# Performance work log

Hardware: AMD Instinct MI355X
Metric: run time of the kernel (lower is better)

## Reference

```python
import jax, jax.numpy as jnp
import numpy as np

D = 32
H = 64
B, N, M = 2, 512, 512


def setup_inputs() -> dict:
    key = jax.random.key(0)
    ks = jax.random.split(key, 6)
    s = 0.1  # modest init scale for MLP params
    return {
        "Q": jax.random.normal(ks[0], (B, N, D), dtype=jnp.float32),
        "K": jax.random.normal(ks[1], (B, M, D), dtype=jnp.float32),
        "w1": jax.random.normal(ks[2], (D, H), dtype=jnp.float32) * s,
        "b1": jax.random.normal(ks[3], (H,), dtype=jnp.float32) * s,
        "w2": jax.random.normal(ks[4], (H, D * D), dtype=jnp.float32) * s,
        "b2": jax.random.normal(ks[5], (D * D,), dtype=jnp.float32) * s,
    }


def _cholesky_factor(x, w1, b1, w2, b2):
    """L(x) with unit-ish softplus diagonal; x: [..., D] -> L: [..., D, D]."""
    h = jax.nn.silu(x @ w1 + b1)
    raw = h @ w2 + b2                      # [..., D*D]
    raw = 5.0 * jnp.tanh(raw / 5.0)        # soft clamp
    L = (raw + jnp.eye(D, dtype=x.dtype).reshape(-1)).reshape(x.shape[:-1] + (D, D))
    tril = jnp.tril(jnp.ones((D, D), dtype=x.dtype))
    diag = jnp.eye(D, dtype=x.dtype)
    L = L * tril
    L = L * (1.0 - diag) + (jax.nn.softplus(L) + 1e-4) * diag
    return L


def reference(Q, K, w1, b1, w2, b2):
    L_q = _cholesky_factor(Q, w1, b1, w2, b2)   # [B,N,D,D]
    L_k = _cholesky_factor(K, w1, b1, w2, b2)   # [B,M,D,D]
    delta = Q[:, :, None, :] - K[:, None, :, :]  # [B,N,M,D]
    # delta^T G_avg delta = 0.5 (||L_q^T delta||^2 + ||L_k^T delta||^2)
    vq = jnp.einsum('bnij,bnmi->bnmj', L_q, delta)  # L_q^T delta
    vk = jnp.einsum('bmij,bnmi->bnmj', L_k, delta)  # L_k^T delta
    dist_sq = 0.5 * (jnp.sum(vq * vq, axis=-1) + jnp.sum(vk * vk, axis=-1))
    return jnp.sqrt(jnp.clip(dist_sq, 1e-6, 1e6))
```

## Files before the change

kernel.cpp:

```cpp
#include <hip/hip_runtime.h>
#include <math.h>

namespace {
constexpr int KF  = 1152;
constexpr int RPB = 4;
}

typedef __bf16 v8bf __attribute__((ext_vector_type(8)));
typedef float  v4f  __attribute__((ext_vector_type(4)));

__device__ __forceinline__ unsigned short f2bf(float f) {
    union { float f; unsigned u; } v; v.f = f;
    unsigned r = v.u + 0x7FFFu + ((v.u >> 16) & 1u);
    return (unsigned short)(r >> 16);
}

__device__ __forceinline__ v8bf as_v8bf(uint4 u) {
    union { uint4 u; v8bf b; } c; c.u = u; return c.b;
}

__global__ __launch_bounds__(256) void k_feat(
    const float* __restrict__ Q, const float* __restrict__ K,
    const float* __restrict__ w1, const float* __restrict__ b1,
    const float* __restrict__ w2, const float* __restrict__ b2,
    unsigned short* __restrict__ featA, unsigned short* __restrict__ featB,
    float* __restrict__ cOut)
{
    __shared__ __attribute__((aligned(16))) float x_s[RPB][32];
    __shared__ __attribute__((aligned(16))) float h_s[RPB][64];
    __shared__ __attribute__((aligned(16))) float L_s[RPB][32][36];
    __shared__ __attribute__((aligned(16))) float G_s[RPB][528];
    __shared__ __attribute__((aligned(16))) float u_s[RPB][32];
    __shared__ unsigned short tri_s[528];

    const int t  = threadIdx.x;
    const int g0 = blockIdx.x * RPB;

    for (int pr = t; pr < 528; pr += 256) {
        int j = (int)((65.0f - sqrtf(4225.0f - 8.0f * (float)pr)) * 0.5f);
        while (j > 0 && j * (65 - j) / 2 > pr) --j;
        while ((j + 1) * (64 - j) / 2 <= pr) ++j;
        int i = j + (pr - j * (65 - j) / 2);
        tri_s[pr] = (unsigned short)((i << 8) | j);
    }
    if (t < RPB * 32) {
        int r = t >> 5, i = t & 31;
        int g = g0 + r;
        const float* src = (g < 1024) ? (Q + (size_t)g * 32)
                                      : (K + (size_t)(g - 1024) * 32);
        x_s[r][i] = src[i];
    }
    __syncthreads();

    {
        int r = t >> 6, j = t & 63;
        float z = b1[j];
        #pragma unroll
        for (int i = 0; i < 32; ++i) z = fmaf(x_s[r][i], w1[i * 64 + j], z);
        h_s[r][j] = z / (1.0f + __expf(-z));
    }
    __syncthreads();

    {
        const int p4 = t * 4;
        float acc[RPB][4];
        float4 bq = *(const float4*)&b2[p4];
        #pragma unroll
        for (int r = 0; r < RPB; ++r) {
            acc[r][0] = bq.x; acc[r][1] = bq.y; acc[r][2] = bq.z; acc[r][3] = bq.w;
        }
        for (int jb = 0; jb < 8; ++jb) {
            float h8[RPB][8];
            #pragma unroll
            for (int r = 0; r < RPB; ++r) {
                *(float4*)&h8[r][0] = *(const float4*)&h_s[r][jb * 8 + 0];
                *(float4*)&h8[r][4] = *(const float4*)&h_s[r][jb * 8 + 4];
            }
            #pragma unroll
            for (int jj = 0; jj < 8; ++jj) {
                float4 w = *(const float4*)&w2[(size_t)(jb * 8 + jj) * 1024 + p4];
                #pragma unroll
                for (int r = 0; r < RPB; ++r) {
                    acc[r][0] = fmaf(h8[r][jj], w.x, acc[r][0]);
                    acc[r][1] = fmaf(h8[r][jj], w.y, acc[r][1]);
                    acc[r][2] = fmaf(h8[r][jj], w.z, acc[r][2]);
                    acc[r][3] = fmaf(h8[r][jj], w.w, acc[r][3]);
                }
            }
        }
        const int i  = p4 >> 5;
        const int j0 = p4 & 31;
        #pragma unroll
        for (int r = 0; r < RPB; ++r) {
            float4 lv;
            float* lvp = (float*)&lv;
            #pragma unroll
            for (int e = 0; e < 4; ++e) {
                int j = j0 + e;
                float raw = acc[r][e];
                float ex = __expf(0.4f * raw);
                float c5 = 5.0f * (ex - 1.0f) / (ex + 1.0f);
                float val;
                if (i < j)       val = 0.0f;
                else if (i == j) { float z = c5 + 1.0f; val = log1pf(__expf(z)) + 1e-4f; }
                else             val = c5;
                lvp[e] = val;
            }
            *(float4*)&L_s[r][i][j0] = lv;
        }
    }
    __syncthreads();

    for (int idx = t; idx < RPB * 528; idx += 256) {
        int r  = idx / 528;
        int pr = idx - r * 528;
        int tv = tri_s[pr];
        int i = tv >> 8, j = tv & 255;
        const float* Li = &L_s[r][i][0];
        const float* Lj = &L_s[r][j][0];
        float s = 0.0f;
        int nf = (j + 1) >> 2;
        for (int q = 0; q < nf; ++q) {
            float4 a  = *(const float4*)&Li[q * 4];
            float4 bb = *(const float4*)&Lj[q * 4];
            s += a.x * bb.x + a.y * bb.y + a.z * bb.z + a.w * bb.w;
        }
        for (int tt = nf * 4; tt <= j; ++tt) s = fmaf(Li[tt], Lj[tt], s);
        G_s[r][pr] = s;
    }
    __syncthreads();

    if (t < RPB * 32) {
        int r = t >> 5, i = t & 31;
        float s = 0.0f;
        #pragma unroll
        for (int j = 0; j < 32; ++j) {
            float gv = (j <= i) ? G_s[r][j * (65 - j) / 2 + i - j]
                                : G_s[r][i * (65 - i) / 2 + j - i];
            s = fmaf(gv, x_s[r][j], s);
        }
        u_s[r][i] = s;
    }
    __syncthreads();

    if (t < RPB) {
        float s = 0.0f;
        #pragma unroll
        for (int i = 0; i < 32; ++i) s = fmaf(u_s[t][i], x_s[t][i], s);
        cOut[g0 + t] = s;
    }

    for (int idx = t; idx < RPB * (KF / 4); idx += 256) {
        int r   = idx / (KF / 4);
        int q   = idx - r * (KF / 4);
        int pos = q * 4;
        int g   = g0 + r;
        bool isA = (g < 1024);
        unsigned short* dst = isA ? (featA + (size_t)g * KF)
                                  : (featB + (size_t)(g - 1024) * KF);
        unsigned short ev[4];
        #pragma unroll
        for (int e = 0; e < 4; ++e) {
            int p = pos + e;
            float va;
            if (p < 1056) {
                int pr = (p < 528) ? p : p - 528;
                bool wantG = (p < 528) ? isA : !isA;
                int tv = tri_s[pr];
                int i = tv >> 8, j = tv & 255;
                float gv = G_s[r][pr] * ((i == j) ? 1.0f : 2.0f);
                float ov = x_s[r][i] * x_s[r][j];
                va = wantG ? gv : ov;
            } else if (p < 1088) {
                int i = p - 1056;
                va = isA ? u_s[r][i] : -2.0f * x_s[r][i];
            } else if (p < 1120) {
                int i = p - 1088;
                va = isA ? x_s[r][i] : -2.0f * u_s[r][i];
            } else {
                va = 0.0f;
            }
            ev[e] = f2bf(va);
        }
        uint2 w;
        w.x = (unsigned)ev[0] | ((unsigned)ev[1] << 16);
        w.y = (unsigned)ev[2] | ((unsigned)ev[3] << 16);
        *(uint2*)(dst + pos) = w;
    }
}

__global__ __launch_bounds__(64) void k_gemm(
    const unsigned short* __restrict__ featA,
    const unsigned short* __restrict__ featB,
    const float* __restrict__ cOut,
    float* __restrict__ out)
{
    const int lane = threadIdx.x;
    const int m0 = blockIdx.x * 32;
    const int n0 = blockIdx.y * 32;
    const int b  = blockIdx.z;
    const int fr = lane & 15;
    const int fq = lane >> 4;

    const unsigned short* pA0 = featA + (size_t)(b * 512 + n0 + fr) * KF + fq * 8;
    const unsigned short* pA1 = pA0 + (size_t)16 * KF;
    const unsigned short* pB0 = featB + (size_t)(b * 512 + m0 + fr) * KF + fq * 8;
    const unsigned short* pB1 = pB0 + (size_t)16 * KF;

    v4f acc00 = {0,0,0,0}, acc01 = {0,0,0,0}, acc10 = {0,0,0,0}, acc11 = {0,0,0,0};

    uint4 bA0[3], bA1[3], bB0[3], bB1[3];
    #pragma unroll
    for (int s = 0; s < 3; ++s) {
        bA0[s] = *(const uint4*)(pA0 + s * 32);
        bA1[s] = *(const uint4*)(pA1 + s * 32);
        bB0[s] = *(const uint4*)(pB0 + s * 32);
        bB1[s] = *(const uint4*)(pB1 + s * 32);
    }

    for (int ks = 0; ks < 36; ks += 3) {
        #pragma unroll
        for (int s = 0; s < 3; ++s) {
            v8bf a0  = as_v8bf(bA0[s]);
            v8bf a1  = as_v8bf(bA1[s]);
            v8bf b0v = as_v8bf(bB0[s]);
            v8bf b1v = as_v8bf(bB1[s]);
            int kn = ks + s + 3;
            if (kn < 36) {
                bA0[s] = *(const uint4*)(pA0 + kn * 32);
                bA1[s] = *(const uint4*)(pA1 + kn * 32);
                bB0[s] = *(const uint4*)(pB0 + kn * 32);
                bB1[s] = *(const uint4*)(pB1 + kn * 32);
            }
            acc00 = __builtin_amdgcn_mfma_f32_16x16x32_bf16(a0, b0v, acc00, 0, 0, 0);
            acc01 = __builtin_amdgcn_mfma_f32_16x16x32_bf16(a0, b1v, acc01, 0, 0, 0);
            acc10 = __builtin_amdgcn_mfma_f32_16x16x32_bf16(a1, b0v, acc10, 0, 0, 0);
            acc11 = __builtin_amdgcn_mfma_f32_16x16x32_bf16(a1, b1v, acc11, 0, 0, 0);
        }
    }

    const int colm = lane & 15;
    const float cB_0 = cOut[1024 + b * 512 + m0 + colm];
    const float cB_1 = cOut[1024 + b * 512 + m0 + 16 + colm];
    const int rbase = lane >> 4;
    #pragma unroll
    for (int v = 0; v < 4; ++v) {
        int n_lo = n0 + rbase * 4 + v;
        int n_hi = n_lo + 16;
        float cA_lo = cOut[b * 512 + n_lo];
        float cA_hi = cOut[b * 512 + n_hi];
        float vv[4] = { acc00[v], acc01[v], acc10[v], acc11[v] };
        int   nn[4] = { n_lo, n_lo, n_hi, n_hi };
        int   mm[4] = { m0 + colm, m0 + 16 + colm, m0 + colm, m0 + 16 + colm };
        float cc[4] = { cA_lo + cB_0, cA_lo + cB_1, cA_hi + cB_0, cA_hi + cB_1 };
        #pragma unroll
        for (int e = 0; e < 4; ++e) {
            float dsq = 0.5f * (vv[e] + cc[e]);
            dsq = fminf(fmaxf(dsq, 1e-6f), 1e6f);
            out[((size_t)(b * 512 + nn[e])) * 512 + mm[e]] = sqrtf(dsq);
        }
    }
}

extern "C" void kernel_launch(void* const* d_in, const int* in_sizes, int n_in,
                              void* d_out, int out_size, void* d_ws, size_t ws_size,
                              hipStream_t stream)
{
    const float* Q  = (const float*)d_in[0];
    const float* K  = (const float*)d_in[1];
    const float* w1 = (const float*)d_in[2];
    const float* b1 = (const float*)d_in[3];
    const float* w2 = (const float*)d_in[4];
    const float* b2 = (const float*)d_in[5];
    float* out = (float*)d_out;

    unsigned short* featA = (unsigned short*)d_ws;
    unsigned short* featB = featA + (size_t)1024 * KF;
    float* cOut = (float*)(featB + (size_t)1024 * KF);

    k_feat<<<dim3(2048 / RPB), dim3(256), 0, stream>>>(Q, K, w1, b1, w2, b2, featA, featB, cOut);
    k_gemm<<<dim3(16, 16, 2), dim3(64), 0, stream>>>(featA, featB, cOut, out);
}
```

Measured before the change: 103.9 us.

## Split K across four waves per block with LDS reduction and swizzled tiles

```diff
diff --git a/kernel.cpp b/kernel.cpp
--- a/kernel.cpp
+++ b/kernel.cpp
@@ -189,77 +189,100 @@
     }
 }
 
-__global__ __launch_bounds__(64) void k_gemm(
+__global__ __launch_bounds__(256) void k_gemm(
     const unsigned short* __restrict__ featA,
     const unsigned short* __restrict__ featB,
     const float* __restrict__ cOut,
     float* __restrict__ out)
 {
-    const int lane = threadIdx.x;
-    const int m0 = blockIdx.x * 32;
-    const int n0 = blockIdx.y * 32;
-    const int b  = blockIdx.z;
+    __shared__ __attribute__((aligned(16))) float red[4][32][36];
+
+    const int t    = threadIdx.x;
+    const int lane = t & 63;
+    const int w    = t >> 6;
+
+    const int lin = blockIdx.x;
+    const int swz = (lin & 7) * 64 + (lin >> 3);
+    const int m0 = (swz & 15) * 32;
+    const int n0 = ((swz >> 4) & 15) * 32;
+    const int b  = swz >> 8;
+
     const int fr = lane & 15;
     const int fq = lane >> 4;
-
-    const unsigned short* pA0 = featA + (size_t)(b * 512 + n0 + fr) * KF + fq * 8;
+    const int kbase = w * 288 + fq * 8;
+
+    const unsigned short* pA0 = featA + (size_t)(b * 512 + n0 + fr) * KF + kbase;
     const unsigned short* pA1 = pA0 + (size_t)16 * KF;
-    const unsigned short* pB0 = featB + (size_t)(b * 512 + m0 + fr) * KF + fq * 8;
+    const unsigned short* pB0 = featB + (size_t)(b * 512 + m0 + fr) * KF + kbase;
     const unsigned short* pB1 = pB0 + (size_t)16 * KF;
 
     v4f acc00 = {0,0,0,0}, acc01 = {0,0,0,0}, acc10 = {0,0,0,0}, acc11 = {0,0,0,0};
 
-    uint4 bA0[3], bA1[3], bB0[3], bB1[3];
+    uint4 bA0[4], bA1[4], bB0[4], bB1[4];
     #pragma unroll
-    for (int s = 0; s < 3; ++s) {
+    for (int s = 0; s < 4; ++s) {
         bA0[s] = *(const uint4*)(pA0 + s * 32);
         bA1[s] = *(const uint4*)(pA1 + s * 32);
         bB0[s] = *(const uint4*)(pB0 + s * 32);
         bB1[s] = *(const uint4*)(pB1 + s * 32);
     }
 
-    for (int ks = 0; ks < 36; ks += 3) {
-        #pragma unroll
-        for (int s = 0; s < 3; ++s) {
-            v8bf a0  = as_v8bf(bA0[s]);
-            v8bf a1  = as_v8bf(bA1[s]);
-            v8bf b0v = as_v8bf(bB0[s]);
-            v8bf b1v = as_v8bf(bB1[s]);
-            int kn = ks + s + 3;
-            if (kn < 36) {
-                bA0[s] = *(const uint4*)(pA0 + kn * 32);
-                bA1[s] = *(const uint4*)(pA1 + kn * 32);
-                bB0[s] = *(const uint4*)(pB0 + kn * 32);
-                bB1[s] = *(const uint4*)(pB1 + kn * 32);
-            }
-            acc00 = __builtin_amdgcn_mfma_f32_16x16x32_bf16(a0, b0v, acc00, 0, 0, 0);
-            acc01 = __builtin_amdgcn_mfma_f32_16x16x32_bf16(a0, b1v, acc01, 0, 0, 0);
-            acc10 = __builtin_amdgcn_mfma_f32_16x16x32_bf16(a1, b0v, acc10, 0, 0, 0);
-            acc11 = __builtin_amdgcn_mfma_f32_16x16x32_bf16(a1, b1v, acc11, 0, 0, 0);
-        }
-    }
-
-    const int colm = lane & 15;
-    const float cB_0 = cOut[1024 + b * 512 + m0 + colm];
-    const float cB_1 = cOut[1024 + b * 512 + m0 + 16 + colm];
-    const int rbase = lane >> 4;
+    #pragma unroll
+    for (int s = 0; s < 9; ++s) {
+        const int slot = s & 3;
+        v8bf a0  = as_v8bf(bA0[slot]);
+        v8bf a1  = as_v8bf(bA1[slot]);
+        v8bf b0v = as_v8bf(bB0[slot]);
+        v8bf b1v = as_v8bf(bB1[slot]);
+        const int kn = s + 4;
+        if (kn < 9) {
+            bA0[slot] = *(const uint4*)(pA0 + kn * 32);
+            bA1[slot] = *(const uint4*)(pA1 + kn * 32);
+            bB0[slot] = *(const uint4*)(pB0 + kn * 32);
+            bB1[slot] = *(const uint4*)(pB1 + kn * 32);
+        }
+        acc00 = __builtin_amdgcn_mfma_f32_16x16x32_bf16(a0, b0v, acc00, 0, 0, 0);
+        acc01 = __builtin_amdgcn_mfma_f32_16x16x32_bf16(a0, b1v, acc01, 0, 0, 0);
+        acc10 = __builtin_amdgcn_mfma_f32_16x16x32_bf16(a1, b0v, acc10, 0, 0, 0);
+        acc11 = __builtin_amdgcn_mfma_f32_16x16x32_bf16(a1, b1v, acc11, 0, 0, 0);
+    }
+
     #pragma unroll
     for (int v = 0; v < 4; ++v) {
-        int n_lo = n0 + rbase * 4 + v;
-        int n_hi = n_lo + 16;
-        float cA_lo = cOut[b * 512 + n_lo];
-        float cA_hi = cOut[b * 512 + n_hi];
-        float vv[4] = { acc00[v], acc01[v], acc10[v], acc11[v] };
-        int   nn[4] = { n_lo, n_lo, n_hi, n_hi };
-        int   mm[4] = { m0 + colm, m0 + 16 + colm, m0 + colm, m0 + 16 + colm };
-        float cc[4] = { cA_lo + cB_0, cA_lo + cB_1, cA_hi + cB_0, cA_hi + cB_1 };
+        red[w][fq * 4 + v][fr]           = acc00[v];
+        red[w][fq * 4 + v][fr + 16]      = acc01[v];
+        red[w][16 + fq * 4 + v][fr]      = acc10[v];
+        red[w][16 + fq * 4 + v][fr + 16] = acc11[v];
+    }
+    __syncthreads();
+
+    const int n_l  = t >> 3;
+    const int m_l0 = (t & 7) * 4;
+    float4 s0 = *(const float4*)&red[0][n_l][m_l0];
+    float4 s1 = *(const float4*)&red[1][n_l][m_l0];
+    float4 s2 = *(const float4*)&red[2][n_l][m_l0];
+    float4 s3 = *(const float4*)&red[3][n_l][m_l0];
+
+    const int   n_g = n0 + n_l;
+    const float cA  = cOut[b * 512 + n_g];
+    const float4 cB = *(const float4*)&cOut[1024 + b * 512 + m0 + m_l0];
+
+    float4 res;
+    {
+        float tot[4] = { s0.x + s1.x + s2.x + s3.x,
+                         s0.y + s1.y + s2.y + s3.y,
+                         s0.z + s1.z + s2.z + s3.z,
+                         s0.w + s1.w + s2.w + s3.w };
+        const float cb[4] = { cB.x, cB.y, cB.z, cB.w };
+        float* rp = (float*)&res;
         #pragma unroll
         for (int e = 0; e < 4; ++e) {
-            float dsq = 0.5f * (vv[e] + cc[e]);
+            float dsq = 0.5f * (tot[e] + cA + cb[e]);
             dsq = fminf(fmaxf(dsq, 1e-6f), 1e6f);
-            out[((size_t)(b * 512 + nn[e])) * 512 + mm[e]] = sqrtf(dsq);
-        }
-    }
+            rp[e] = sqrtf(dsq);
+        }
+    }
+    *(float4*)&out[((size_t)(b * 512 + n_g)) * 512 + m0 + m_l0] = res;
 }
 
 extern "C" void kernel_launch(void* const* d_in, const int* in_sizes, int n_in,
@@ -279,5 +302,5 @@
     float* cOut = (float*)(featB + (size_t)1024 * KF);
 
     k_feat<<<dim3(2048 / RPB), dim3(256), 0, stream>>>(Q, K, w1, b1, w2, b2, featA, featB, cOut);
-    k_gemm<<<dim3(16, 16, 2), dim3(64), 0, stream>>>(featA, featB, cOut, out);
-}
+    k_gemm<<<dim3(512), dim3(256), 0, stream>>>(featA, featB, cOut, out);
+}
```

Measured after the change: 101.1 us. 1.03x faster.
